# Optimization experiments

Hardware: AMD Instinct MI355X
Metric: run time of the kernel (lower is better)

## Reference

```python
import jax, jax.numpy as jnp
import numpy as np

D = 128  # chunk_embSize

def _mlp_one_layer(x, W, b):
    # MLP_one_layer in eval mode: dropout is identity -> tanh(x @ W^T + b)
    return jnp.tanh(x @ W.T + b)

def setup_inputs() -> dict:
    key = jax.random.key(0)
    ks = jax.random.split(key, 10)
    n_item, n_opi, n_user, L = 50000, 5000, 10000, 50
    s = 0.02  # initializer_range-style scale for linear weights
    return {
        "item_table": jax.random.normal(ks[0], (n_item, D), jnp.float32),
        "opin_table": jax.random.normal(ks[1], (n_opi, D), jnp.float32),
        "user_emb": jax.random.normal(ks[2], (n_user, D), jnp.float32),
        "attr_embedding": jax.random.normal(ks[3], (D,), jnp.float32),
        "Wq": jax.random.normal(ks[4], (D, D), jnp.float32) * s,
        "bq": jnp.zeros((D,), jnp.float32),
        "Wk": jax.random.normal(ks[5], (D, D), jnp.float32) * s,
        "bk": jnp.zeros((D,), jnp.float32),
        "Wv": jax.random.normal(ks[6], (D, D), jnp.float32) * s,
        "bv": jnp.zeros((D,), jnp.float32),
        "item_seqs": jax.random.randint(ks[7], (n_user, L), 0, n_item, jnp.int64),
        "opin_seqs": jax.random.randint(ks[8], (n_user, L), 0, n_opi, jnp.int64),
    }

def reference(item_table, opin_table, user_emb, attr_embedding,
              Wq, bq, Wk, bk, Wv, bv, item_seqs, opin_seqs):
    # FineRec UiMatrix.opin_update_ui (eval mode: all dropouts identity)
    item_emb = item_table[item_seqs]          # [U, L, D] gather
    opin_emb = opin_table[opin_seqs]          # [U, L, D] gather
    # k = k_layer(attr + item); v = v_layer(item + opin); q = q_layer(user)
    k_emb = _mlp_one_layer(attr_embedding[None, None, :] + item_emb, Wk, bk)
    v_emb = _mlp_one_layer(item_emb + opin_emb, Wv, bv)
    q_emb = _mlp_one_layer(user_emb, Wq, bq)  # [U, D]
    # unnormalized attention weights over the user's interaction sequence
    w_agg = jnp.einsum("ud,uld->ul", q_emb, k_emb)  # [U, L]
    mask = (item_seqs > 0).astype(w_agg.dtype)       # padding mask
    w_agg = w_agg * mask
    # weighted aggregation over sequence -> new user embedding
    user_embedding = jnp.einsum("ul,uld->ud", w_agg, v_emb)  # [U, D]
    return user_embedding
```

## Files before the change

kernel.cpp:

```cpp
#include <hip/hip_runtime.h>
#include <hip/hip_bf16.h>
#include <stdint.h>

typedef __attribute__((ext_vector_type(8))) short bf16x8;
typedef __attribute__((ext_vector_type(4))) float f32x4;

#define S_2LOG2E 2.8853900817779268f

#if __has_builtin(__builtin_amdgcn_exp2f)
#define EXP2F(x) __builtin_amdgcn_exp2f(x)
#else
#define EXP2F(x) __expf((x) * 0.6931471805599453f)
#endif
#if __has_builtin(__builtin_amdgcn_rcpf)
#define RCPF(x) __builtin_amdgcn_rcpf(x)
#else
#define RCPF(x) (1.0f / (x))
#endif

__device__ __forceinline__ float tanh_z(float z) {
    float e = EXP2F(z);
    float r = RCPF(e + 1.0f);
    return fmaf(-2.0f, r, 1.0f);
}
__device__ __forceinline__ float tanh_fast(float x) {
    float e = __expf(2.0f * x);
    return 1.0f - 2.0f / (e + 1.0f);
}

__device__ __forceinline__ bf16x8 pack2(float4 a, float4 b) {
    union { bf16x8 v; __hip_bfloat162 h[4]; } r;
    r.h[0] = __float22bfloat162_rn(make_float2(a.x, a.y));
    r.h[1] = __float22bfloat162_rn(make_float2(a.z, a.w));
    r.h[2] = __float22bfloat162_rn(make_float2(b.x, b.y));
    r.h[3] = __float22bfloat162_rn(make_float2(b.z, b.w));
    return r.v;
}
__device__ __forceinline__ float4 scl4(float4 a) {
    a.x *= S_2LOG2E; a.y *= S_2LOG2E; a.z *= S_2LOG2E; a.w *= S_2LOG2E;
    return a;
}
#define MFMA16(a, b, c) __builtin_amdgcn_mfma_f32_16x16x32_bf16((a), (b), (c), 0, 0, 0)

__global__ void finerec_prep(
    const float* __restrict__ user_emb, const float* __restrict__ attr,
    const float* __restrict__ Wq, const float* __restrict__ bq,
    const float* __restrict__ Wk, const float* __restrict__ bk,
    const float* __restrict__ Wv, const float* __restrict__ bv,
    const float* __restrict__ item_table, const float* __restrict__ opin_table,
    float* __restrict__ q_ws, float* __restrict__ bkz_ws, float* __restrict__ bvz_ws,
    short* __restrict__ wf_ws, short* __restrict__ itb, short* __restrict__ opb,
    float* __restrict__ out, int U, int n_item, int n_opi, int qb)
{
    const int bx = blockIdx.x, tid = threadIdx.x;
    if (bx >= qb + 49) {
        const int castb = gridDim.x - qb - 49;
        const int gid = (bx - qb - 49) * 256 + tid;
        const int stride = castb * 256;
        const int tci = n_item * 16, tc = (n_item + n_opi) * 16;
        for (int c = gid; c < tc; c += stride) {
            if (c < tci) {
                const float* src = item_table + (size_t)c * 8;
                ((bf16x8*)itb)[c] = pack2(*(const float4*)src, *(const float4*)(src + 4));
            } else {
                const float* src = opin_table + (size_t)(c - tci) * 8;
                ((bf16x8*)opb)[c - tci] = pack2(*(const float4*)src, *(const float4*)(src + 4));
            }
        }
        return;
    }
    if (bx >= qb + 9) {
        const int gid = (bx - qb - 9) * 256 + tid;
        float4 z = {0.0f, 0.0f, 0.0f, 0.0f};
        for (int i = gid; i < U * 32; i += 40 * 256) ((float4*)out)[i] = z;
        return;
    }
    if (bx >= qb + 1) {
        const int bi = bx - qb - 1;
#pragma unroll
        for (int t = 0; t < 2; ++t) {
            const int g = bi * 512 + t * 256 + tid;
            const int mat = g >> 11, gg = g & 2047, r = gg >> 4, c = gg & 15;
            const float* src = (mat ? Wv : Wk) + r * 128 + c * 8;
            ((bf16x8*)wf_ws)[(mat << 11) + (r << 4) + (c ^ (r & 15))] =
                pack2(scl4(*(const float4*)src), scl4(*(const float4*)(src + 4)));
        }
        return;
    }
    if (bx == qb) {
        if (tid < 128) {
            const float* wr = Wk + tid * 128;
            float s = bk[tid];
            for (int k = 0; k < 128; k += 4) {
                float4 w4 = *(const float4*)(wr + k);
                float4 a4 = *(const float4*)(attr + k);
                s += w4.x * a4.x + w4.y * a4.y + w4.z * a4.z + w4.w * a4.w;
            }
            bkz_ws[tid] = s * S_2LOG2E;
        } else if (tid < 256) {
            bvz_ws[tid - 128] = bv[tid - 128] * S_2LOG2E;
        }
        return;
    }
    const int wv = tid >> 6, lane = tid & 63;
    const int l15 = lane & 15, quad = lane >> 4;
    const int u0 = (bx * 4 + wv) * 16;
    int ur = u0 + l15; if (ur >= U) ur = U - 1;
    const float* up = user_emb + (size_t)ur * 128 + quad * 8;
    bf16x8 af[4];
#pragma unroll
    for (int ks = 0; ks < 4; ++ks)
        af[ks] = pack2(*(const float4*)(up + ks * 32), *(const float4*)(up + ks * 32 + 4));
#pragma unroll
    for (int nt = 0; nt < 8; ++nt) {
        const int n = nt * 16 + l15;
        const float* wp = Wq + n * 128 + quad * 8;
        f32x4 acc = {0, 0, 0, 0};
#pragma unroll
        for (int ks = 0; ks < 4; ++ks) {
            bf16x8 bf = pack2(*(const float4*)(wp + ks * 32), *(const float4*)(wp + ks * 32 + 4));
            acc = MFMA16(af[ks], bf, acc);
        }
        const float bqv = bq[n];
#pragma unroll
        for (int r = 0; r < 4; ++r) {
            int row = u0 + quad * 4 + r;
            if (row < U) q_ws[row * 128 + nt * 16 + l15] = tanh_fast(acc[r] + bqv);
        }
    }
}

template<int BF16, int LC>
__global__ __launch_bounds__(1024, 4) void finerec_main(
    const float* __restrict__ item_table, const float* __restrict__ opin_table,
    const int* __restrict__ item_seqs, const int* __restrict__ opin_seqs,
    const float* __restrict__ q_ws, const float* __restrict__ bkz_ws,
    const float* __restrict__ bvz_ws, const short* __restrict__ wf_ws,
    const short* __restrict__ itb, const short* __restrict__ opb,
    float* __restrict__ out, int U, int Lrt)
{
    __shared__ __align__(16) short wlds[32768];
    __shared__ float bkz_lds[128], bvz_lds[128];

    const int L = LC ? LC : Lrt;
    const int tid = threadIdx.x;
    const int wv = tid >> 6, lane = tid & 63, l15 = lane & 15, quad = lane >> 4;

    const bf16x8* wsrc = (const bf16x8*)wf_ws;
    bf16x8* wldsv = (bf16x8*)wlds;
#pragma unroll
    for (int i = 0; i < 4; ++i)
        wldsv[i * 1024 + tid] = wsrc[i * 1024 + tid];
    if (tid < 128)      bkz_lds[tid]       = bkz_ws[tid];
    else if (tid < 256) bvz_lds[tid - 128] = bvz_ws[tid - 128];
    __syncthreads();

    const int UL = U * L;
    const int njobs = (UL + 15) >> 4;
    const int nwaves = gridDim.x * 16;

#pragma unroll 1
    for (int job = blockIdx.x * 16 + wv; job < njobs; job += nwaves) {
        const int g0 = job << 4;
        const int uA = g0 / L;
        const int bb = L - (g0 - uA * L);
        const bool split = (bb < 16) && (uA + 1 < U);

        int vi = 0, vo = 0;
        if (lane < 16 && g0 + lane < UL) {
            vi = item_seqs[g0 + lane];
            vo = opin_seqs[g0 + lane];
        }
        const unsigned long long mb = __ballot(vi > 0);

        const int idx = __shfl(vi, l15);
        bf16x8 ai[4];
        if (BF16) {
            const bf16x8* pb = (const bf16x8*)itb + (size_t)idx * 16 + quad;
#pragma unroll
            for (int ks = 0; ks < 4; ++ks) ai[ks] = pb[ks * 4];
        } else {
            const float* p = item_table + (size_t)idx * 128 + quad * 8;
#pragma unroll
            for (int ks = 0; ks < 4; ++ks)
                ai[ks] = pack2(*(const float4*)(p + ks * 32), *(const float4*)(p + ks * 32 + 4));
        }
        const int od = __shfl(vo, l15);
        bf16x8 ao[4];
        if (BF16) {
            const bf16x8* pb = (const bf16x8*)opb + (size_t)od * 16 + quad;
#pragma unroll
            for (int ks = 0; ks < 4; ++ks) ao[ks] = pb[ks * 4];
        } else {
            const float* p = opin_table + (size_t)od * 128 + quad * 8;
#pragma unroll
            for (int ks = 0; ks < 4; ++ks)
                ao[ks] = pack2(*(const float4*)(p + ks * 32), *(const float4*)(p + ks * 32 + 4));
        }

        const float* qpA = q_ws + (size_t)uA * 128;
        float w[4] = {0, 0, 0, 0};

        if (!split) {
#pragma unroll 1
            for (int nt = 0; nt < 8; ++nt) {
                const int n = nt * 16 + l15;
                const float qa = qpA[n];
                const float bz = bkz_lds[n];
                f32x4 c = {bz, bz, bz, bz};
#pragma unroll
                for (int ks = 0; ks < 4; ++ks)
                    c = MFMA16(ai[ks], wldsv[(n << 4) + ((ks * 4 + quad) ^ l15)], c);
#pragma unroll
                for (int r = 0; r < 4; ++r)
                    w[r] = fmaf(qa, tanh_z(c[r]), w[r]);
            }
        } else {
            const float* qpB = qpA + 128;
#pragma unroll 1
            for (int nt = 0; nt < 8; ++nt) {
                const int n = nt * 16 + l15;
                const float qa = qpA[n];
                const float qb2 = qpB[n];
                const float bz = bkz_lds[n];
                f32x4 c = {bz, bz, bz, bz};
#pragma unroll
                for (int ks = 0; ks < 4; ++ks)
                    c = MFMA16(ai[ks], wldsv[(n << 4) + ((ks * 4 + quad) ^ l15)], c);
#pragma unroll
                for (int r = 0; r < 4; ++r) {
                    const float qv = (quad * 4 + r < bb) ? qa : qb2;
                    w[r] = fmaf(qv, tanh_z(c[r]), w[r]);
                }
            }
        }
#pragma unroll
        for (int r = 0; r < 4; ++r) {
            float t = w[r];
            t += __shfl_xor(t, 1); t += __shfl_xor(t, 2);
            t += __shfl_xor(t, 4); t += __shfl_xor(t, 8);
            w[r] = ((mb >> (quad * 4 + r)) & 1ull) ? t : 0.0f;
        }
        float* op = out + (size_t)uA * 128 + quad * 32 + l15;
        if (!split) {
            float s0 = 0.0f, s1 = 0.0f;
#pragma unroll 1
            for (int nt = 0; nt < 8; ++nt) {
                const int n = nt * 16 + l15;
                const float bz = bvz_lds[n];
                f32x4 c = {bz, bz, bz, bz};
#pragma unroll
                for (int ks = 0; ks < 4; ++ks) {
                    const bf16x8 wf = wldsv[2048 + (n << 4) + ((ks * 4 + quad) ^ l15)];
                    c = MFMA16(ai[ks], wf, c);
                    c = MFMA16(ao[ks], wf, c);
                }
                float acc = 0.0f;
#pragma unroll
                for (int r = 0; r < 4; ++r)
                    acc = fmaf(w[r], tanh_z(c[r]), acc);
                acc += __shfl_xor(acc, 16);
                acc += __shfl_xor(acc, 32);
                const bool mine = (quad == (nt >> 1));
                s0 += (mine && !(nt & 1)) ? acc : 0.0f;
                s1 += (mine &&  (nt & 1)) ? acc : 0.0f;
            }
            atomicAdd(op, s0);
            atomicAdd(op + 16, s1);
        } else {
            float sA0 = 0.0f, sA1 = 0.0f, sB0 = 0.0f, sB1 = 0.0f;
#pragma unroll 1
            for (int nt = 0; nt < 8; ++nt) {
                const int n = nt * 16 + l15;
                const float bz = bvz_lds[n];
                f32x4 c = {bz, bz, bz, bz};
#pragma unroll
                for (int ks = 0; ks < 4; ++ks) {
                    const bf16x8 wf = wldsv[2048 + (n << 4) + ((ks * 4 + quad) ^ l15)];
                    c = MFMA16(ai[ks], wf, c);
                    c = MFMA16(ao[ks], wf, c);
                }
                float accT = 0.0f, accA = 0.0f;
#pragma unroll
                for (int r = 0; r < 4; ++r) {
                    const float t = w[r] * tanh_z(c[r]);
                    accT += t;
                    accA += (quad * 4 + r < bb) ? t : 0.0f;
                }
                accT += __shfl_xor(accT, 16); accT += __shfl_xor(accT, 32);
                accA += __shfl_xor(accA, 16); accA += __shfl_xor(accA, 32);
                const float accB = accT - accA;
                const bool mine = (quad == (nt >> 1));
                const bool lo = !(nt & 1);
                sA0 += (mine && lo)  ? accA : 0.0f;
                sA1 += (mine && !lo) ? accA : 0.0f;
                sB0 += (mine && lo)  ? accB : 0.0f;
                sB1 += (mine && !lo) ? accB : 0.0f;
            }
            atomicAdd(op, sA0);
            atomicAdd(op + 16, sA1);
            atomicAdd(op + 128, sB0);
            atomicAdd(op + 144, sB1);
        }
    }
}

extern "C" void kernel_launch(void* const* d_in, const int* in_sizes, int n_in,
                              void* d_out, int out_size, void* d_ws, size_t ws_size,
                              hipStream_t stream) {
    const float* item_table = (const float*)d_in[0];
    const float* opin_table = (const float*)d_in[1];
    const float* user_emb   = (const float*)d_in[2];
    const float* attr       = (const float*)d_in[3];
    const float* Wq = (const float*)d_in[4];
    const float* bq = (const float*)d_in[5];
    const float* Wk = (const float*)d_in[6];
    const float* bk = (const float*)d_in[7];
    const float* Wv = (const float*)d_in[8];
    const float* bv = (const float*)d_in[9];
    const int* item_seqs = (const int*)d_in[10];
    const int* opin_seqs = (const int*)d_in[11];
    float* out = (float*)d_out;

    const int U = in_sizes[2] / 128;
    const int L = in_sizes[10] / U;
    const int n_item = in_sizes[0] / 128;
    const int n_opi  = in_sizes[1] / 128;

    char* w = (char*)d_ws;
    float* q_ws   = (float*)w;               w += (size_t)U * 128 * 4;
    float* bkz_ws = (float*)w;               w += 512;
    float* bvz_ws = (float*)w;               w += 512;
    short* wf_ws  = (short*)w;               w += 4096 * 16;
    short* itb    = (short*)w;               w += (size_t)n_item * 128 * 2;
    short* opb    = (short*)w;               w += (size_t)n_opi * 128 * 2;
    const size_t need = (size_t)(w - (char*)d_ws);
    const int use_bf16 = (ws_size >= need) ? 1 : 0;

    const int qb = (U + 63) / 64;
    const int castb = use_bf16 ? (((n_item + n_opi) * 16 + 255) / 256) : 0;
    const int prep_grid = qb + 49 + castb;
    finerec_prep<<<prep_grid, 256, 0, stream>>>(
        user_emb, attr, Wq, bq, Wk, bk, Wv, bv, item_table, opin_table,
        q_ws, bkz_ws, bvz_ws, wf_ws, itb, opb, out, U, n_item, n_opi, qb);

    if (use_bf16) {
        if (L == 50)
            finerec_main<1, 50><<<512, 1024, 0, stream>>>(
                item_table, opin_table, item_seqs, opin_seqs,
                q_ws, bkz_ws, bvz_ws, wf_ws, itb, opb, out, U, L);
        else
            finerec_main<1, 0><<<512, 1024, 0, stream>>>(
                item_table, opin_table, item_seqs, opin_seqs,
                q_ws, bkz_ws, bvz_ws, wf_ws, itb, opb, out, U, L);
    } else {
        if (L == 50)
            finerec_main<0, 50><<<512, 1024, 0, stream>>>(
                item_table, opin_table, item_seqs, opin_seqs,
                q_ws, bkz_ws, bvz_ws, wf_ws, itb, opb, out, U, L);
        else
            finerec_main<0, 0><<<512, 1024, 0, stream>>>(
                item_table, opin_table, item_seqs, opin_seqs,
                q_ws, bkz_ws, bvz_ws, wf_ws, itb, opb, out, U, L);
    }
}
```

Before: 184.3 us.

## Precompute per-table K activations and V projections, reducing main kernel to gathers

Uses linearity of the V projection and the per-item nature of K: the prep kernel now computes tanh(Wk(item+attr)+bk) and Wv·item for every item row, plus Wv·opin for every opinion row, storing them in bf16. The main kernel then gathers these rows and does only a dot product with q and a tanh over summed projections, with no per-interaction MFMA. This replaces 500k per-interaction GEMM rows with 55k table-row GEMMs. It costs larger workspace (item rows double width) and adds extra bf16 rounding of intermediate projections before the tanh.

```diff
diff --git a/kernel.cpp b/kernel.cpp
--- a/kernel.cpp
+++ b/kernel.cpp
@@ -40,6 +40,21 @@
     a.x *= S_2LOG2E; a.y *= S_2LOG2E; a.z *= S_2LOG2E; a.w *= S_2LOG2E;
     return a;
 }
+__device__ __forceinline__ float4 add4(float4 a, float4 b) {
+    return make_float4(a.x + b.x, a.y + b.y, a.z + b.z, a.w + b.w);
+}
+__device__ __forceinline__ unsigned short f2bf(float x) {
+    __hip_bfloat16 h = __float2bfloat16(x);
+    return *reinterpret_cast<unsigned short*>(&h);
+}
+__device__ __forceinline__ void bf8f(bf16x8 v, float* f) {
+    union { bf16x8 v; unsigned u[4]; } a; a.v = v;
+#pragma unroll
+    for (int i = 0; i < 4; ++i) {
+        f[2 * i]     = __uint_as_float(a.u[i] << 16);
+        f[2 * i + 1] = __uint_as_float(a.u[i] & 0xffff0000u);
+    }
+}
 #define MFMA16(a, b, c) __builtin_amdgcn_mfma_f32_16x16x32_bf16((a), (b), (c), 0, 0, 0)
 
 __global__ void finerec_prep(
@@ -49,22 +64,68 @@
     const float* __restrict__ Wv, const float* __restrict__ bv,
     const float* __restrict__ item_table, const float* __restrict__ opin_table,
     float* __restrict__ q_ws, float* __restrict__ bkz_ws, float* __restrict__ bvz_ws,
-    short* __restrict__ wf_ws, short* __restrict__ itb, short* __restrict__ opb,
+    short* __restrict__ wf_ws, short* __restrict__ cit, short* __restrict__ po_t,
     float* __restrict__ out, int U, int n_item, int n_opi, int qb)
 {
     const int bx = blockIdx.x, tid = threadIdx.x;
-    if (bx >= qb + 49) {
-        const int castb = gridDim.x - qb - 49;
-        const int gid = (bx - qb - 49) * 256 + tid;
-        const int stride = castb * 256;
-        const int tci = n_item * 16, tc = (n_item + n_opi) * 16;
-        for (int c = gid; c < tc; c += stride) {
-            if (c < tci) {
-                const float* src = item_table + (size_t)c * 8;
-                ((bf16x8*)itb)[c] = pack2(*(const float4*)src, *(const float4*)(src + 4));
-            } else {
-                const float* src = opin_table + (size_t)(c - tci) * 8;
-                ((bf16x8*)opb)[c - tci] = pack2(*(const float4*)src, *(const float4*)(src + 4));
+    const int cb0 = qb + 49;
+    if (bx >= cb0) {
+        const int citb = (n_item + 63) >> 6;
+        const int wvp = tid >> 6, lane = tid & 63;
+        const int l15 = lane & 15, quad = lane >> 4;
+        const bool isPo = bx >= cb0 + citb;
+        const int sj = ((bx - (isPo ? cb0 + citb : cb0)) << 2) + wvp;
+        const int r0 = sj << 4;
+        const int nrows = isPo ? n_opi : n_item;
+        if (r0 >= nrows) return;
+        const float* tbl = isPo ? opin_table : item_table;
+        int ur = r0 + l15; if (ur >= nrows) ur = nrows - 1;
+        const float* rp = tbl + (size_t)ur * 128 + quad * 8;
+        bf16x8 afK[4], afV[4];
+#pragma unroll
+        for (int ks = 0; ks < 4; ++ks) {
+            float4 ia = *(const float4*)(rp + ks * 32);
+            float4 ib = *(const float4*)(rp + ks * 32 + 4);
+            afV[ks] = pack2(ia, ib);
+            if (!isPo) {
+                float4 aa = *(const float4*)(attr + quad * 8 + ks * 32);
+                float4 ab = *(const float4*)(attr + quad * 8 + ks * 32 + 4);
+                afK[ks] = pack2(add4(ia, aa), add4(ib, ab));
+            }
+        }
+#pragma unroll 1
+        for (int nt = 0; nt < 8; ++nt) {
+            const int n = nt * 16 + l15;
+            f32x4 cV = {0, 0, 0, 0};
+            f32x4 cK = {0, 0, 0, 0};
+            if (!isPo) {
+                const float bzk = bk[n] * S_2LOG2E;
+                cK = (f32x4){bzk, bzk, bzk, bzk};
+            }
+#pragma unroll
+            for (int ks = 0; ks < 4; ++ks) {
+                const int co = (ks * 4 + quad) * 8;
+                const float* wvpp = Wv + n * 128 + co;
+                bf16x8 bV = pack2(scl4(*(const float4*)wvpp), scl4(*(const float4*)(wvpp + 4)));
+                cV = MFMA16(afV[ks], bV, cV);
+                if (!isPo) {
+                    const float* wkp = Wk + n * 128 + co;
+                    bf16x8 bK = pack2(scl4(*(const float4*)wkp), scl4(*(const float4*)(wkp + 4)));
+                    cK = MFMA16(afK[ks], bK, cK);
+                }
+            }
+#pragma unroll
+            for (int r = 0; r < 4; ++r) {
+                const int row = r0 + quad * 4 + r;
+                if (row < nrows) {
+                    if (isPo) {
+                        ((unsigned short*)po_t)[(size_t)row * 128 + n] = f2bf(cV[r]);
+                    } else {
+                        unsigned short* crow = (unsigned short*)cit + (size_t)row * 256;
+                        crow[n]       = f2bf(tanh_z(cK[r]));
+                        crow[128 + n] = f2bf(cV[r]);
+                    }
+                }
             }
         }
         return;
@@ -130,13 +191,129 @@
     }
 }
 
-template<int BF16, int LC>
+template<int LC>
+__global__ __launch_bounds__(1024) void finerec_main2(
+    const int* __restrict__ item_seqs, const int* __restrict__ opin_seqs,
+    const float* __restrict__ q_ws, const float* __restrict__ bvz_ws,
+    const short* __restrict__ cit, const short* __restrict__ po_t,
+    float* __restrict__ out, int U, int Lrt)
+{
+    const int L = LC ? LC : Lrt;
+    const int tid = threadIdx.x;
+    const int wv = tid >> 6, lane = tid & 63, l15 = lane & 15, quad = lane >> 4;
+    const int UL = U * L;
+    const int njobs = (UL + 15) >> 4;
+    const int nwaves = gridDim.x * 16;
+
+    float bz[8];
+    {
+        float4 b0 = *(const float4*)(bvz_ws + l15 * 8);
+        float4 b1 = *(const float4*)(bvz_ws + l15 * 8 + 4);
+        bz[0] = b0.x; bz[1] = b0.y; bz[2] = b0.z; bz[3] = b0.w;
+        bz[4] = b1.x; bz[5] = b1.y; bz[6] = b1.z; bz[7] = b1.w;
+    }
+
+#pragma unroll 1
+    for (int job = blockIdx.x * 16 + wv; job < njobs; job += nwaves) {
+        const int g0 = job << 4;
+        const int uA = g0 / L;
+        const int bb = L - (g0 - uA * L);
+        const bool split = (bb < 16);
+
+        int vi = 0, vo = 0;
+        if (lane < 16 && g0 + lane < UL) {
+            vi = item_seqs[g0 + lane];
+            vo = opin_seqs[g0 + lane];
+        }
+        const unsigned long long mb = __ballot(vi > 0);
+
+        const int idx = __shfl(vi, l15);
+        const int qrow = (l15 < bb) ? uA : uA + 1;
+        const float* qp = q_ws + (size_t)qrow * 128 + quad * 32;
+        const bf16x8* kp = (const bf16x8*)cit + (size_t)idx * 32 + quad * 4;
+        float dot = 0.0f;
+#pragma unroll
+        for (int ks = 0; ks < 4; ++ks) {
+            float kf[8]; bf8f(kp[ks], kf);
+            const float4 qa = *(const float4*)(qp + ks * 8);
+            const float4 qb4 = *(const float4*)(qp + ks * 8 + 4);
+            dot = fmaf(kf[0], qa.x, dot);  dot = fmaf(kf[1], qa.y, dot);
+            dot = fmaf(kf[2], qa.z, dot);  dot = fmaf(kf[3], qa.w, dot);
+            dot = fmaf(kf[4], qb4.x, dot); dot = fmaf(kf[5], qb4.y, dot);
+            dot = fmaf(kf[6], qb4.z, dot); dot = fmaf(kf[7], qb4.w, dot);
+        }
+        dot += __shfl_xor(dot, 16);
+        dot += __shfl_xor(dot, 32);
+        const float wrow = ((mb >> l15) & 1ull) ? dot : 0.0f;
+
+        float* op = out + (size_t)uA * 128 + l15 * 8 + quad * 2;
+        if (!split) {
+            float acc[8] = {0, 0, 0, 0, 0, 0, 0, 0};
+#pragma unroll
+            for (int r = 0; r < 4; ++r) {
+                const int rw = quad * 4 + r;
+                const float wv_ = __shfl(wrow, rw);
+                const int ir = __shfl(vi, rw);
+                const int orr = __shfl(vo, rw);
+                float pf[8], of[8];
+                bf8f(*((const bf16x8*)cit + (size_t)ir * 32 + 16 + l15), pf);
+                bf8f(*((const bf16x8*)po_t + (size_t)orr * 16 + l15), of);
+#pragma unroll
+                for (int j = 0; j < 8; ++j)
+                    acc[j] = fmaf(wv_, tanh_z(pf[j] + of[j] + bz[j]), acc[j]);
+            }
+#pragma unroll
+            for (int j = 0; j < 8; ++j) {
+                acc[j] += __shfl_xor(acc[j], 16);
+                acc[j] += __shfl_xor(acc[j], 32);
+            }
+            const float v0 = quad == 0 ? acc[0] : quad == 1 ? acc[2] : quad == 2 ? acc[4] : acc[6];
+            const float v1 = quad == 0 ? acc[1] : quad == 1 ? acc[3] : quad == 2 ? acc[5] : acc[7];
+            atomicAdd(op, v0);
+            atomicAdd(op + 1, v1);
+        } else {
+            float accT[8] = {0, 0, 0, 0, 0, 0, 0, 0};
+            float accA[8] = {0, 0, 0, 0, 0, 0, 0, 0};
+#pragma unroll
+            for (int r = 0; r < 4; ++r) {
+                const int rw = quad * 4 + r;
+                const float wv_ = __shfl(wrow, rw);
+                const float wvA = (rw < bb) ? wv_ : 0.0f;
+                const int ir = __shfl(vi, rw);
+                const int orr = __shfl(vo, rw);
+                float pf[8], of[8];
+                bf8f(*((const bf16x8*)cit + (size_t)ir * 32 + 16 + l15), pf);
+                bf8f(*((const bf16x8*)po_t + (size_t)orr * 16 + l15), of);
+#pragma unroll
+                for (int j = 0; j < 8; ++j) {
+                    const float t = tanh_z(pf[j] + of[j] + bz[j]);
+                    accT[j] = fmaf(wv_, t, accT[j]);
+                    accA[j] = fmaf(wvA, t, accA[j]);
+                }
+            }
+#pragma unroll
+            for (int j = 0; j < 8; ++j) {
+                accT[j] += __shfl_xor(accT[j], 16); accT[j] += __shfl_xor(accT[j], 32);
+                accA[j] += __shfl_xor(accA[j], 16); accA[j] += __shfl_xor(accA[j], 32);
+            }
+            const float a0 = quad == 0 ? accA[0] : quad == 1 ? accA[2] : quad == 2 ? accA[4] : accA[6];
+            const float a1 = quad == 0 ? accA[1] : quad == 1 ? accA[3] : quad == 2 ? accA[5] : accA[7];
+            const float t0 = quad == 0 ? accT[0] : quad == 1 ? accT[2] : quad == 2 ? accT[4] : accT[6];
+            const float t1 = quad == 0 ? accT[1] : quad == 1 ? accT[3] : quad == 2 ? accT[5] : accT[7];
+            atomicAdd(op, a0);
+            atomicAdd(op + 1, a1);
+            atomicAdd(op + 128, t0 - a0);
+            atomicAdd(op + 129, t1 - a1);
+        }
+    }
+}
+
+template<int LC>
 __global__ __launch_bounds__(1024, 4) void finerec_main(
     const float* __restrict__ item_table, const float* __restrict__ opin_table,
     const int* __restrict__ item_seqs, const int* __restrict__ opin_seqs,
     const float* __restrict__ q_ws, const float* __restrict__ bkz_ws,
     const float* __restrict__ bvz_ws, const short* __restrict__ wf_ws,
-    const short* __restrict__ itb, const short* __restrict__ opb,
     float* __restrict__ out, int U, int Lrt)
 {
     __shared__ __align__(16) short wlds[32768];
@@ -175,39 +352,21 @@
 
         const int idx = __shfl(vi, l15);
         bf16x8 ai[4];
-        if (BF16) {
-            const bf16x8* pb = (const bf16x8*)itb + (size_t)idx * 16 + quad;
-#pragma unroll
-            for (int ks = 0; ks < 4; ++ks) ai[ks] = pb[ks * 4];
-        } else {
+        {
             const float* p = item_table + (size_t)idx * 128 + quad * 8;
 #pragma unroll
             for (int ks = 0; ks < 4; ++ks)
                 ai[ks] = pack2(*(const float4*)(p + ks * 32), *(const float4*)(p + ks * 32 + 4));
         }
-        const int od = __shfl(vo, l15);
-        bf16x8 ao[4];
-        if (BF16) {
-            const bf16x8* pb = (const bf16x8*)opb + (size_t)od * 16 + quad;
-#pragma unroll
-            for (int ks = 0; ks < 4; ++ks) ao[ks] = pb[ks * 4];
-        } else {
-            const float* p = opin_table + (size_t)od * 128 + quad * 8;
-#pragma unroll
-            for (int ks = 0; ks < 4; ++ks)
-                ao[ks] = pack2(*(const float4*)(p + ks * 32), *(const float4*)(p + ks * 32 + 4));
-        }
-
         const float* qpA = q_ws + (size_t)uA * 128;
         float w[4] = {0, 0, 0, 0};
-
         if (!split) {
 #pragma unroll 1
             for (int nt = 0; nt < 8; ++nt) {
                 const int n = nt * 16 + l15;
                 const float qa = qpA[n];
-                const float bz = bkz_lds[n];
-                f32x4 c = {bz, bz, bz, bz};
+                const float bzv = bkz_lds[n];
+                f32x4 c = {bzv, bzv, bzv, bzv};
 #pragma unroll
                 for (int ks = 0; ks < 4; ++ks)
                     c = MFMA16(ai[ks], wldsv[(n << 4) + ((ks * 4 + quad) ^ l15)], c);
@@ -222,8 +381,8 @@
                 const int n = nt * 16 + l15;
                 const float qa = qpA[n];
                 const float qb2 = qpB[n];
-                const float bz = bkz_lds[n];
-                f32x4 c = {bz, bz, bz, bz};
+                const float bzv = bkz_lds[n];
+                f32x4 c = {bzv, bzv, bzv, bzv};
 #pragma unroll
                 for (int ks = 0; ks < 4; ++ks)
                     c = MFMA16(ai[ks], wldsv[(n << 4) + ((ks * 4 + quad) ^ l15)], c);
@@ -241,14 +400,22 @@
             t += __shfl_xor(t, 4); t += __shfl_xor(t, 8);
             w[r] = ((mb >> (quad * 4 + r)) & 1ull) ? t : 0.0f;
         }
+        const int od = __shfl(vo, l15);
+        bf16x8 ao[4];
+        {
+            const float* p = opin_table + (size_t)od * 128 + quad * 8;
+#pragma unroll
+            for (int ks = 0; ks < 4; ++ks)
+                ao[ks] = pack2(*(const float4*)(p + ks * 32), *(const float4*)(p + ks * 32 + 4));
+        }
         float* op = out + (size_t)uA * 128 + quad * 32 + l15;
         if (!split) {
             float s0 = 0.0f, s1 = 0.0f;
 #pragma unroll 1
             for (int nt = 0; nt < 8; ++nt) {
                 const int n = nt * 16 + l15;
-                const float bz = bvz_lds[n];
-                f32x4 c = {bz, bz, bz, bz};
+                const float bzv = bvz_lds[n];
+                f32x4 c = {bzv, bzv, bzv, bzv};
 #pragma unroll
                 for (int ks = 0; ks < 4; ++ks) {
                     const bf16x8 wf = wldsv[2048 + (n << 4) + ((ks * 4 + quad) ^ l15)];
@@ -272,8 +439,8 @@
 #pragma unroll 1
             for (int nt = 0; nt < 8; ++nt) {
                 const int n = nt * 16 + l15;
-                const float bz = bvz_lds[n];
-                f32x4 c = {bz, bz, bz, bz};
+                const float bzv = bvz_lds[n];
+                f32x4 c = {bzv, bzv, bzv, bzv};
 #pragma unroll
                 for (int ks = 0; ks < 4; ++ks) {
                     const bf16x8 wf = wldsv[2048 + (n << 4) + ((ks * 4 + quad) ^ l15)];
@@ -332,35 +499,34 @@
     float* bkz_ws = (float*)w;               w += 512;
     float* bvz_ws = (float*)w;               w += 512;
     short* wf_ws  = (short*)w;               w += 4096 * 16;
-    short* itb    = (short*)w;               w += (size_t)n_item * 128 * 2;
-    short* opb    = (short*)w;               w += (size_t)n_opi * 128 * 2;
-    const size_t need = (size_t)(w - (char*)d_ws);
-    const int use_bf16 = (ws_size >= need) ? 1 : 0;
+    short* cit    = (short*)w;               w += (size_t)n_item * 256 * 2;
+    short* po_t   = (short*)w;               w += (size_t)n_opi * 128 * 2;
+    const size_t need_new = (size_t)(w - (char*)d_ws);
+    const int use_new = (ws_size >= need_new) ? 1 : 0;
 
     const int qb = (U + 63) / 64;
-    const int castb = use_bf16 ? (((n_item + n_opi) * 16 + 255) / 256) : 0;
-    const int prep_grid = qb + 49 + castb;
+    const int citb = (n_item + 63) / 64;
+    const int pob  = (n_opi + 63) / 64;
+    const int prep_grid = qb + 49 + (use_new ? (citb + pob) : 0);
     finerec_prep<<<prep_grid, 256, 0, stream>>>(
         user_emb, attr, Wq, bq, Wk, bk, Wv, bv, item_table, opin_table,
-        q_ws, bkz_ws, bvz_ws, wf_ws, itb, opb, out, U, n_item, n_opi, qb);
-
-    if (use_bf16) {
+        q_ws, bkz_ws, bvz_ws, wf_ws, cit, po_t, out, U, n_item, n_opi, qb);
+
+    if (use_new) {
         if (L == 50)
-            finerec_main<1, 50><<<512, 1024, 0, stream>>>(
-                item_table, opin_table, item_seqs, opin_seqs,
-                q_ws, bkz_ws, bvz_ws, wf_ws, itb, opb, out, U, L);
+            finerec_main2<50><<<512, 1024, 0, stream>>>(
+                item_seqs, opin_seqs, q_ws, bvz_ws, cit, po_t, out, U, L);
         else
-            finerec_main<1, 0><<<512, 1024, 0, stream>>>(
-                item_table, opin_table, item_seqs, opin_seqs,
-                q_ws, bkz_ws, bvz_ws, wf_ws, itb, opb, out, U, L);
+            finerec_main2<0><<<512, 1024, 0, stream>>>(
+                item_seqs, opin_seqs, q_ws, bvz_ws, cit, po_t, out, U, L);
     } else {
         if (L == 50)
-            finerec_main<0, 50><<<512, 1024, 0, stream>>>(
+            finerec_main<50><<<512, 1024, 0, stream>>>(
                 item_table, opin_table, item_seqs, opin_seqs,
-                q_ws, bkz_ws, bvz_ws, wf_ws, itb, opb, out, U, L);
+                q_ws, bkz_ws, bvz_ws, wf_ws, out, U, L);
         else
-            finerec_main<0, 0><<<512, 1024, 0, stream>>>(
+            finerec_main<0><<<512, 1024, 0, stream>>>(
                 item_table, opin_table, item_seqs, opin_seqs,
-                q_ws, bkz_ws, bvz_ws, wf_ws, itb, opb, out, U, L);
-    }
-}
+                q_ws, bkz_ws, bvz_ws, wf_ws, out, U, L);
+    }
+}
```

New measurement: 209.9 us. 1.14x slower.
